# Performance work log

Measured on AMD Instinct MI355X. Metric: run time of the kernel, lower is better.

The kernel has to match this reference:

```python
import jax, jax.numpy as jnp
import numpy as np

EPS = 1e-5


def setup_inputs() -> dict:
    key = jax.random.key(0)
    ks = jax.random.split(key, 8)
    B, C, D, H, O, E = 256, 64, 256, 4096, 256, 4
    x = jax.random.normal(ks[0], (B, C, D), dtype=jnp.float32)
    mask_ids = jax.random.randint(ks[1], (B, C), 0, 16)
    projection_idx = jax.random.randint(ks[2], (C,), 0, E)
    W1 = jax.random.normal(ks[3], (E, D, H), dtype=jnp.float32) * 0.02
    b1 = jnp.zeros((E, H), dtype=jnp.float32)
    gamma = jnp.ones((E, H), dtype=jnp.float32)
    beta = jnp.zeros((E, H), dtype=jnp.float32)
    W2 = jax.random.normal(ks[4], (E, H, O), dtype=jnp.float32) * 0.02
    b2 = jnp.zeros((E, O), dtype=jnp.float32)
    return {"x": x, "mask_ids": mask_ids, "projection_idx": projection_idx,
            "W1": W1, "b1": b1, "gamma": gamma, "beta": beta, "W2": W2, "b2": b2}


def reference(x, mask_ids, projection_idx, W1, b1, gamma, beta, W2, b2):
    # x: [B, C, D]; projection_idx: [C] routes each channel to one of E experts.
    # Disjoint masks => the original zeros + masked '+=' is a partition-assign.
    B, C, D = x.shape
    E, _, H = W1.shape
    # Per-channel expert params (gather once, shared over batch).
    h = jnp.einsum('bcd,cdh->bch', x, W1[projection_idx]) + b1[projection_idx]
    # BatchNorm1d in training mode: batch stats over the tokens of each expert
    # (the original flattens the selected [B, |mask|] tokens for BN).
    seg = jnp.broadcast_to(projection_idx[None, :], (B, C)).reshape(-1)  # [B*C]
    hf = h.reshape(B * C, H)
    cnt = jax.ops.segment_sum(jnp.ones((B * C,), h.dtype), seg, num_segments=E)
    cnt = jnp.maximum(cnt, 1.0)
    s1 = jax.ops.segment_sum(hf, seg, num_segments=E)            # [E, H]
    s2 = jax.ops.segment_sum(hf * hf, seg, num_segments=E)       # [E, H]
    mean = s1 / cnt[:, None]
    var = s2 / cnt[:, None] - mean * mean                        # biased var (train-mode BN)
    inv = jax.lax.rsqrt(var + EPS)
    hn = (h - mean[projection_idx]) * (inv[projection_idx] * gamma[projection_idx]) + beta[projection_idx]
    a = jax.nn.relu(hn)
    out = jnp.einsum('bch,cho->bco', a, W2[projection_idx]) + b2[projection_idx]
    return out, mask_ids
```

## Files before the change

### kernel.cpp

```cpp
#include <hip/hip_runtime.h>

typedef unsigned short u16;
typedef unsigned int   u32;
typedef __attribute__((ext_vector_type(8))) short s16x8;
typedef __attribute__((ext_vector_type(4))) float f32x4;
typedef __attribute__((ext_vector_type(4))) u32   u32x4;

#define DEV static __device__ __forceinline__

static constexpr int B_ = 256, C_ = 64, D_ = 256, H_ = 4096, O_ = 256, E_ = 4;

DEV u16 f2bf(float f) {
  u32 u = __builtin_bit_cast(u32, f);
  u += 0x7fffu + ((u >> 16) & 1u);
  return (u16)(u >> 16);
}
DEV float bf2f(u16 u) { return __builtin_bit_cast(float, (u32)u << 16); }

DEV void async16(const u16* g, u16* l) {
  __builtin_amdgcn_global_load_lds(
      (const __attribute__((address_space(1))) void*)g,
      (__attribute__((address_space(3))) void*)l, 16, 0, 0);
}

DEV int xcd_swz(int bid, int nwg) { return (bid & 7) * (nwg >> 3) + (bid >> 3); }

__global__ void k_cvt(const float* __restrict__ src, u16* __restrict__ dst) {
  const int i = blockIdx.x * blockDim.x + threadIdx.x;
  const f32x4 a = ((const f32x4*)src)[2 * i];
  const f32x4 b = ((const f32x4*)src)[2 * i + 1];
  u32x4 o;
  o[0] = (u32)f2bf(a[0]) | ((u32)f2bf(a[1]) << 16);
  o[1] = (u32)f2bf(a[2]) | ((u32)f2bf(a[3]) << 16);
  o[2] = (u32)f2bf(b[0]) | ((u32)f2bf(b[1]) << 16);
  o[3] = (u32)f2bf(b[2]) | ((u32)f2bf(b[3]) << 16);
  ((u32x4*)dst)[i] = o;
}

__global__ void k_transpose(const float* __restrict__ src, u16* __restrict__ dst,
                            const int R, const int Cc) {
  __shared__ float tile[64][65];
  const int nct = Cc >> 6, nrt = R >> 6;
  int bx = blockIdx.x;
  const int ct = bx % nct; bx /= nct;
  const int rt = bx % nrt; const int e = bx / nrt;
  const float* s = src + (size_t)e * R * Cc;
  u16* d = dst + (size_t)e * R * Cc;
  const int tx = threadIdx.x & 63, ty = threadIdx.x >> 6;
  #pragma unroll
  for (int i = 0; i < 64; i += 4)
    tile[i + ty][tx] = s[(size_t)(rt * 64 + i + ty) * Cc + ct * 64 + tx];
  __syncthreads();
  #pragma unroll
  for (int i = 0; i < 64; i += 4) {
    const int cc = i + ty;
    d[(size_t)(ct * 64 + cc) * R + rt * 64 + tx] = f2bf(tile[tx][cc]);
  }
}

__global__ void k_sortc(const int* __restrict__ proj, int* __restrict__ perm) {
  const int c = threadIdx.x;
  const int e = proj[c];
  int rank = 0;
  for (int c2 = 0; c2 < C_; ++c2) {
    const int e2 = proj[c2];
    rank += (e2 < e) || (e2 == e && c2 < c);
  }
  perm[rank] = c;
}

__global__ __launch_bounds__(256, 4)
void k_gemm1(const u16* __restrict__ A, const u16* __restrict__ Bw,
             const int* __restrict__ proj, const int* __restrict__ perm,
             const float* __restrict__ bias,
             u16* __restrict__ outH, float* __restrict__ s1g, float* __restrict__ s2g) {
  constexpr int BM = 128, BN = 128, BK = 32, KT = D_ / BK;
  constexpr int SA = BM * BK / 8, SB = BN * BK / 8;
  constexpr int BUF = (SA + SB) * 8;
  __shared__ __align__(16) u16 lds[2 * BUF];
  const int tid = threadIdx.x, l = tid & 63, w = tid >> 6, wm = w >> 1, wn = w & 1;

  int bid = xcd_swz(blockIdx.x, gridDim.x);
  constexpr int NT = H_ / BN, BT = B_ / BM;
  const int nt = bid % NT; bid /= NT;
  const int bt = bid % BT; const int ci = bid / BT;
  const int c = perm[ci];
  const int e = proj[c];

  const size_t rsA = (size_t)C_ * D_;
  const u16* Ab = A + (size_t)c * D_ + (size_t)bt * BM * rsA;
  const u16* Bb = Bw + ((size_t)e * H_ + (size_t)nt * BN) * D_;

  f32x4 acc[4][4] = {};

  auto stage = [&](int kt) {
    const int k0 = kt * BK;
    u16* dst = lds + (kt & 1) * BUF;
    #pragma unroll
    for (int i = 0; i < SA / 256; ++i) {
      const int s = i * 256 + tid, row = s >> 2, j = (s & 3) ^ (row & 3);
      async16(Ab + (size_t)row * rsA + k0 + j * 8, dst + s * 8);
    }
    #pragma unroll
    for (int i = 0; i < SB / 256; ++i) {
      const int s = i * 256 + tid, col = s >> 2, j = (s & 3) ^ (col & 3);
      async16(Bb + (size_t)col * D_ + k0 + j * 8, dst + SA * 8 + s * 8);
    }
  };

  stage(0);
  asm volatile("s_waitcnt vmcnt(0)" ::: "memory");
  __builtin_amdgcn_s_barrier();

  #pragma unroll
  for (int kt = 0; kt < KT; ++kt) {
    if (kt + 1 < KT) stage(kt + 1);
    const u16* bufA = lds + (kt & 1) * BUF;
    const u16* bufB = bufA + SA * 8;
    s16x8 av[4], bv[4];
    #pragma unroll
    for (int m = 0; m < 4; ++m) {
      const int r = wm * 64 + m * 16 + (l & 15), p = (l >> 4) ^ (r & 3);
      av[m] = *(const s16x8*)(bufA + (r * 4 + p) * 8);
    }
    #pragma unroll
    for (int n = 0; n < 4; ++n) {
      const int cc = wn * 64 + n * 16 + (l & 15), p = (l >> 4) ^ (cc & 3);
      bv[n] = *(const s16x8*)(bufB + (cc * 4 + p) * 8);
    }
    #pragma unroll
    for (int m = 0; m < 4; ++m)
      #pragma unroll
      for (int n = 0; n < 4; ++n)
        acc[m][n] = __builtin_amdgcn_mfma_f32_16x16x32_bf16(av[m], bv[n], acc[m][n], 0, 0, 0);
    asm volatile("s_waitcnt vmcnt(0) lgkmcnt(0)" ::: "memory");
    __builtin_amdgcn_s_barrier();
  }

  u16* ldsOut = lds;
  #pragma unroll
  for (int n = 0; n < 4; ++n) {
    const int colL = wn * 64 + n * 16 + (l & 15);
    const int colg = nt * BN + colL;
    const float bval = bias[e * H_ + colg];
    float p1 = 0.f, p2 = 0.f;
    #pragma unroll
    for (int m = 0; m < 4; ++m) {
      const int rbase = wm * 64 + m * 16 + (l >> 4) * 4;
      #pragma unroll
      for (int i = 0; i < 4; ++i) {
        const float v = acc[m][n][i] + bval;
        p1 += v; p2 += v * v;
        const int row = rbase + i;
        const int phys = (colL >> 3) ^ (row & 15);
        ldsOut[row * 128 + phys * 8 + (colL & 7)] = f2bf(v);
      }
    }
    p1 += __shfl_xor(p1, 16); p1 += __shfl_xor(p1, 32);
    p2 += __shfl_xor(p2, 16); p2 += __shfl_xor(p2, 32);
    if (l < 16) {
      atomicAdd(&s1g[e * H_ + colg], p1);
      atomicAdd(&s2g[e * H_ + colg], p2);
    }
  }
  __syncthreads();
  u16* outB = outH + ((size_t)(bt * BM) * C_ + c) * H_ + nt * BN;
  #pragma unroll
  for (int pass = 0; pass < 8; ++pass) {
    const int row = pass * 16 + (tid >> 4), sl = tid & 15;
    const u32x4 v = *(const u32x4*)(ldsOut + row * 128 + ((sl ^ (row & 15)) * 8));
    *(u32x4*)(outB + (size_t)row * C_ * H_ + sl * 8) = v;
  }
}

__global__ void k_finalize(const float* __restrict__ s1, const float* __restrict__ s2,
                           const int* __restrict__ proj, const float* __restrict__ gamma,
                           const float* __restrict__ beta,
                           u16* __restrict__ sclB, u16* __restrict__ shfB) {
  const int i = blockIdx.x * 256 + threadIdx.x;
  const int e = i >> 12;
  int cn = 0;
  #pragma unroll
  for (int c = 0; c < C_; ++c) cn += (proj[c] == e) ? 1 : 0;
  const float cnt = fmaxf((float)cn * (float)B_, 1.f);
  const float mean = s1[i] / cnt;
  const float var = s2[i] / cnt - mean * mean;
  const float sc = rsqrtf(var + 1e-5f) * gamma[i];
  sclB[i] = f2bf(sc);
  shfB[i] = f2bf(beta[i] - mean * sc);
}

__global__ __launch_bounds__(256, 2)
void k_gemm2(const u16* __restrict__ A, const u16* __restrict__ Bw,
             const int* __restrict__ proj, const int* __restrict__ perm,
             const float* __restrict__ b2,
             const u16* __restrict__ scB, const u16* __restrict__ shB,
             float* __restrict__ outF, float* __restrict__ partial) {
  constexpr int BM = 128, BN = 128, BK = 64, KH = H_ / 2, KT = KH / BK;
  constexpr int SA = BM * BK / 8, SB = BN * BK / 8;
  constexpr int BUF = (SA + SB) * 8;
  __shared__ __align__(16) u16 lds[2 * BUF];
  const int tid = threadIdx.x, l = tid & 63, w = tid >> 6, wm = w >> 1, wn = w & 1;

  int bid = xcd_swz(blockIdx.x, gridDim.x);
  const int ks = bid & 1; bid >>= 1;
  const int nt = bid & 1; bid >>= 1;
  const int bt = bid & 1; const int ci = bid >> 1;
  const int c = perm[ci];
  const int e = proj[c];

  const size_t rsA = (size_t)C_ * H_;
  const u16* Ab = A + (size_t)c * H_ + (size_t)bt * BM * rsA + (size_t)ks * KH;
  const u16* Bb = Bw + ((size_t)e * O_ + (size_t)nt * BN) * H_ + (size_t)ks * KH;
  const u16* scE = scB + e * H_ + ks * KH;
  const u16* shE = shB + e * H_ + ks * KH;

  f32x4 acc[4][4] = {};
  s16x8 hA[4], sA[4], tA[4];

  auto Aissue = [&](int kt) {
    const int k0 = kt * BK;
    #pragma unroll
    for (int i = 0; i < 4; ++i) {
      const int s = i * 256 + tid, row = s >> 3, j = (s & 7) ^ (row & 7), k = k0 + j * 8;
      hA[i] = *(const s16x8*)(Ab + (size_t)row * rsA + k);
      sA[i] = *(const s16x8*)(scE + k);
      tA[i] = *(const s16x8*)(shE + k);
    }
  };
  auto Bissue = [&](int kt) {
    const int k0 = kt * BK;
    u16* dst = lds + (kt & 1) * BUF + SA * 8;
    #pragma unroll
    for (int i = 0; i < 4; ++i) {
      const int s = i * 256 + tid, col = s >> 3, j = (s & 7) ^ (col & 7);
      async16(Bb + (size_t)col * H_ + k0 + j * 8, dst + s * 8);
    }
  };
  auto Awrite = [&](int kt) {
    u16* dst = lds + (kt & 1) * BUF;
    #pragma unroll
    for (int i = 0; i < 4; ++i) {
      const int s = i * 256 + tid;
      u32x4 o;
      #pragma unroll
      for (int jj = 0; jj < 4; ++jj) {
        const float v0 = fmaxf(bf2f((u16)hA[i][2 * jj]) * bf2f((u16)sA[i][2 * jj]) + bf2f((u16)tA[i][2 * jj]), 0.f);
        const float v1 = fmaxf(bf2f((u16)hA[i][2 * jj + 1]) * bf2f((u16)sA[i][2 * jj + 1]) + bf2f((u16)tA[i][2 * jj + 1]), 0.f);
        o[jj] = (u32)f2bf(v0) | ((u32)f2bf(v1) << 16);
      }
      *(u32x4*)(dst + s * 8) = o;
    }
  };

  Aissue(0); Bissue(0); Awrite(0);
  asm volatile("s_waitcnt vmcnt(0) lgkmcnt(0)" ::: "memory");
  __builtin_amdgcn_s_barrier();

  #pragma unroll 2
  for (int kt = 0; kt < KT; ++kt) {
    if (kt + 1 < KT) { Aissue(kt + 1); Bissue(kt + 1); }
    const u16* bufA = lds + (kt & 1) * BUF;
    const u16* bufB = bufA + SA * 8;
    s16x8 av[2][4], bv[2][4];
    #pragma unroll
    for (int kk = 0; kk < 2; ++kk) {
      #pragma unroll
      for (int m = 0; m < 4; ++m) {
        const int r = wm * 64 + m * 16 + (l & 15), p = (kk * 4 + (l >> 4)) ^ (r & 7);
        av[kk][m] = *(const s16x8*)(bufA + (r * 8 + p) * 8);
      }
      #pragma unroll
      for (int n = 0; n < 4; ++n) {
        const int cc = wn * 64 + n * 16 + (l & 15), p = (kk * 4 + (l >> 4)) ^ (cc & 7);
        bv[kk][n] = *(const s16x8*)(bufB + (cc * 8 + p) * 8);
      }
    }
    #pragma unroll
    for (int kk = 0; kk < 2; ++kk)
      #pragma unroll
      for (int m = 0; m < 4; ++m)
        #pragma unroll
        for (int n = 0; n < 4; ++n)
          acc[m][n] = __builtin_amdgcn_mfma_f32_16x16x32_bf16(av[kk][m], bv[kk][n], acc[m][n], 0, 0, 0);
    if (kt + 1 < KT) Awrite(kt + 1);
    asm volatile("s_waitcnt vmcnt(0) lgkmcnt(0)" ::: "memory");
    __builtin_amdgcn_s_barrier();
  }

  float* dstF = ks ? partial : outF;
  #pragma unroll
  for (int n = 0; n < 4; ++n) {
    const int colg = nt * BN + wn * 64 + n * 16 + (l & 15);
    const float bval = ks ? 0.f : b2[e * O_ + colg];
    #pragma unroll
    for (int m = 0; m < 4; ++m) {
      #pragma unroll
      for (int i = 0; i < 4; ++i) {
        const int rg = bt * BM + wm * 64 + m * 16 + (l >> 4) * 4 + i;
        dstF[((size_t)rg * C_ + c) * O_ + colg] = acc[m][n][i] + bval;
      }
    }
  }
}

__global__ void k_combine(float* __restrict__ out, const float* __restrict__ partial,
                          const int* __restrict__ mask, float* __restrict__ maskOut) {
  const int gi = blockIdx.x * 256 + threadIdx.x;
  const size_t b = (size_t)gi * 2;
  f32x4 a0 = ((const f32x4*)out)[b],     a1 = ((const f32x4*)out)[b + 1];
  const f32x4 p0 = ((const f32x4*)partial)[b], p1 = ((const f32x4*)partial)[b + 1];
  #pragma unroll
  for (int j = 0; j < 4; ++j) { a0[j] += p0[j]; a1[j] += p1[j]; }
  ((f32x4*)out)[b] = a0; ((f32x4*)out)[b + 1] = a1;
  if (gi < B_ * C_ / 8) {
    #pragma unroll
    for (int j = 0; j < 8; ++j) maskOut[gi * 8 + j] = (float)mask[gi * 8 + j];
  }
}

extern "C" void kernel_launch(void* const* d_in, const int* in_sizes, int n_in,
                              void* d_out, int out_size, void* d_ws, size_t ws_size,
                              hipStream_t stream) {
  const float* x     = (const float*)d_in[0];
  const int*   mask  = (const int*)d_in[1];
  const int*   proj  = (const int*)d_in[2];
  const float* W1    = (const float*)d_in[3];
  const float* b1    = (const float*)d_in[4];
  const float* gamma = (const float*)d_in[5];
  const float* beta  = (const float*)d_in[6];
  const float* W2    = (const float*)d_in[7];
  const float* b2    = (const float*)d_in[8];
  float* out = (float*)d_out;

  char* ws = (char*)d_ws;
  size_t off = 0;
  u16* hbuf = (u16*)(ws + off); off += (size_t)B_ * C_ * H_ * 2;
  u16* xb   = (u16*)(ws + off); off += (size_t)B_ * C_ * D_ * 2;
  u16* w1t  = (u16*)(ws + off); off += (size_t)E_ * D_ * H_ * 2;
  float* partial = (float*)xb;
  u16* w2t  = (u16*)(ws + off); off += (size_t)E_ * H_ * O_ * 2;
  float* s1 = (float*)(ws + off); off += (size_t)E_ * H_ * 4;
  float* s2 = (float*)(ws + off); off += (size_t)E_ * H_ * 4;
  u16* sclB = (u16*)(ws + off); off += (size_t)E_ * H_ * 2;
  u16* shfB = (u16*)(ws + off); off += (size_t)E_ * H_ * 2;
  int* perm = (int*)(ws + off); off += 256;

  (void)hipMemsetAsync(s1, 0, (size_t)2 * E_ * H_ * 4, stream);

  k_sortc<<<1, 64, 0, stream>>>(proj, perm);
  k_cvt<<<2048, 256, 0, stream>>>(x, xb);
  k_transpose<<<E_ * 4 * 64, 256, 0, stream>>>(W1, w1t, D_, H_);
  k_transpose<<<E_ * 64 * 4, 256, 0, stream>>>(W2, w2t, H_, O_);

  k_gemm1<<<C_ * 2 * 32, 256, 0, stream>>>(xb, w1t, proj, perm, b1, hbuf, s1, s2);

  k_finalize<<<E_ * H_ / 256, 256, 0, stream>>>(s1, s2, proj, gamma, beta, sclB, shfB);

  k_gemm2<<<512, 256, 0, stream>>>(hbuf, w2t, proj, perm, b2, sclB, shfB, out, partial);

  k_combine<<<B_ * C_ * O_ / 8 / 256, 256, 0, stream>>>(out, partial, mask,
                                                        out + (size_t)B_ * C_ * O_);
}
```

Measured before the change: 160.3 us.

## Restructure gemm2 into triple-buffered register-staged pipeline with LDS-cached BN scale/shift

The second GEMM now uses a K tile of 32 instead of 64. LDS becomes a three-deep ring buffer. Both A and B tiles are loaded into registers two steps ahead and written to LDS one step ahead, replacing the async global-to-LDS copies for B. The BatchNorm scale and shift vectors for the block's K range are loaded into LDS once, instead of being re-read from global memory on every A load. This is meant to hide global latency behind MFMA work and cut redundant scale/shift traffic, at the cost of more barriers per K and more register pressure. The gemm1 loop bounds are hardcoded to 2, which is presumably equal to the previous constant.

```diff
diff --git a/kernel.cpp b/kernel.cpp
--- a/kernel.cpp
+++ b/kernel.cpp
@@ -97,12 +97,12 @@
     const int k0 = kt * BK;
     u16* dst = lds + (kt & 1) * BUF;
     #pragma unroll
-    for (int i = 0; i < SA / 256; ++i) {
+    for (int i = 0; i < 2; ++i) {
       const int s = i * 256 + tid, row = s >> 2, j = (s & 3) ^ (row & 3);
       async16(Ab + (size_t)row * rsA + k0 + j * 8, dst + s * 8);
     }
     #pragma unroll
-    for (int i = 0; i < SB / 256; ++i) {
+    for (int i = 0; i < 2; ++i) {
       const int s = i * 256 + tid, col = s >> 2, j = (s & 3) ^ (col & 3);
       async16(Bb + (size_t)col * D_ + k0 + j * 8, dst + SA * 8 + s * 8);
     }
@@ -196,10 +196,12 @@
              const float* __restrict__ b2,
              const u16* __restrict__ scB, const u16* __restrict__ shB,
              float* __restrict__ outF, float* __restrict__ partial) {
-  constexpr int BM = 128, BN = 128, BK = 64, KH = H_ / 2, KT = KH / BK;
+  constexpr int BM = 128, BN = 128, BK = 32, KH = H_ / 2, KT = KH / BK;
   constexpr int SA = BM * BK / 8, SB = BN * BK / 8;
   constexpr int BUF = (SA + SB) * 8;
-  __shared__ __align__(16) u16 lds[2 * BUF];
+  __shared__ __align__(16) u16 lds[3 * BUF + 2 * KH];
+  u16* stS = lds + 3 * BUF;
+  u16* stT = stS + KH;
   const int tid = threadIdx.x, l = tid & 63, w = tid >> 6, wm = w >> 1, wn = w & 1;
 
   int bid = xcd_swz(blockIdx.x, gridDim.x);
@@ -216,77 +218,99 @@
   const u16* shE = shB + e * H_ + ks * KH;
 
   f32x4 acc[4][4] = {};
-  s16x8 hA[4], sA[4], tA[4];
-
-  auto Aissue = [&](int kt) {
+  s16x8 h0[2], h1[2], b0r[2], b1r[2];
+
+  auto Aissue = [&](int kt, s16x8 (&hs)[2]) {
     const int k0 = kt * BK;
     #pragma unroll
-    for (int i = 0; i < 4; ++i) {
-      const int s = i * 256 + tid, row = s >> 3, j = (s & 7) ^ (row & 7), k = k0 + j * 8;
-      hA[i] = *(const s16x8*)(Ab + (size_t)row * rsA + k);
-      sA[i] = *(const s16x8*)(scE + k);
-      tA[i] = *(const s16x8*)(shE + k);
-    }
-  };
-  auto Bissue = [&](int kt) {
+    for (int i = 0; i < 2; ++i) {
+      const int s = i * 256 + tid, row = s >> 2, j = (s & 3) ^ (row & 3);
+      hs[i] = *(const s16x8*)(Ab + (size_t)row * rsA + k0 + j * 8);
+    }
+  };
+  auto Bissue = [&](int kt, s16x8 (&bs)[2]) {
     const int k0 = kt * BK;
-    u16* dst = lds + (kt & 1) * BUF + SA * 8;
-    #pragma unroll
-    for (int i = 0; i < 4; ++i) {
-      const int s = i * 256 + tid, col = s >> 3, j = (s & 7) ^ (col & 7);
-      async16(Bb + (size_t)col * H_ + k0 + j * 8, dst + s * 8);
-    }
-  };
-  auto Awrite = [&](int kt) {
-    u16* dst = lds + (kt & 1) * BUF;
-    #pragma unroll
-    for (int i = 0; i < 4; ++i) {
-      const int s = i * 256 + tid;
+    #pragma unroll
+    for (int i = 0; i < 2; ++i) {
+      const int s = i * 256 + tid, col = s >> 2, j = (s & 3) ^ (col & 3);
+      bs[i] = *(const s16x8*)(Bb + (size_t)col * H_ + k0 + j * 8);
+    }
+  };
+  auto Awrite = [&](int kt, s16x8 (&hs)[2]) {
+    u16* dst = lds + (kt % 3) * BUF;
+    const int k0 = kt * BK;
+    #pragma unroll
+    for (int i = 0; i < 2; ++i) {
+      const int s = i * 256 + tid, row = s >> 2, j = (s & 3) ^ (row & 3);
+      const s16x8 sv = *(const s16x8*)(stS + k0 + j * 8);
+      const s16x8 tv = *(const s16x8*)(stT + k0 + j * 8);
       u32x4 o;
       #pragma unroll
       for (int jj = 0; jj < 4; ++jj) {
-        const float v0 = fmaxf(bf2f((u16)hA[i][2 * jj]) * bf2f((u16)sA[i][2 * jj]) + bf2f((u16)tA[i][2 * jj]), 0.f);
-        const float v1 = fmaxf(bf2f((u16)hA[i][2 * jj + 1]) * bf2f((u16)sA[i][2 * jj + 1]) + bf2f((u16)tA[i][2 * jj + 1]), 0.f);
+        const float v0 = fmaxf(bf2f((u16)hs[i][2 * jj]) * bf2f((u16)sv[2 * jj]) + bf2f((u16)tv[2 * jj]), 0.f);
+        const float v1 = fmaxf(bf2f((u16)hs[i][2 * jj + 1]) * bf2f((u16)sv[2 * jj + 1]) + bf2f((u16)tv[2 * jj + 1]), 0.f);
         o[jj] = (u32)f2bf(v0) | ((u32)f2bf(v1) << 16);
       }
       *(u32x4*)(dst + s * 8) = o;
     }
   };
-
-  Aissue(0); Bissue(0); Awrite(0);
-  asm volatile("s_waitcnt vmcnt(0) lgkmcnt(0)" ::: "memory");
+  auto Bwrite = [&](int kt, s16x8 (&bs)[2]) {
+    u16* dst = lds + (kt % 3) * BUF + SA * 8;
+    #pragma unroll
+    for (int i = 0; i < 2; ++i) {
+      const int s = i * 256 + tid;
+      *(u32x4*)(dst + s * 8) = __builtin_bit_cast(u32x4, bs[i]);
+    }
+  };
+  auto Compute = [&](int kt) {
+    const u16* bufA = lds + (kt % 3) * BUF;
+    const u16* bufB = bufA + SA * 8;
+    s16x8 av[4], bv[4];
+    #pragma unroll
+    for (int m = 0; m < 4; ++m) {
+      const int r = wm * 64 + m * 16 + (l & 15), p = (l >> 4) ^ (r & 3);
+      av[m] = *(const s16x8*)(bufA + (r * 4 + p) * 8);
+    }
+    #pragma unroll
+    for (int n = 0; n < 4; ++n) {
+      const int cc = wn * 64 + n * 16 + (l & 15), p = (l >> 4) ^ (cc & 3);
+      bv[n] = *(const s16x8*)(bufB + (cc * 4 + p) * 8);
+    }
+    #pragma unroll
+    for (int m = 0; m < 4; ++m)
+      #pragma unroll
+      for (int n = 0; n < 4; ++n)
+        acc[m][n] = __builtin_amdgcn_mfma_f32_16x16x32_bf16(av[m], bv[n], acc[m][n], 0, 0, 0);
+  };
+
+  async16(scE + tid * 8, stS + tid * 8);
+  async16(shE + tid * 8, stT + tid * 8);
+  Aissue(0, h0); Bissue(0, b0r);
+  Aissue(1, h1); Bissue(1, b1r);
+  asm volatile("s_waitcnt vmcnt(0)" ::: "memory");
+  Awrite(0, h0); Bwrite(0, b0r);
+  asm volatile("s_waitcnt lgkmcnt(0)" ::: "memory");
   __builtin_amdgcn_s_barrier();
 
-  #pragma unroll 2
-  for (int kt = 0; kt < KT; ++kt) {
-    if (kt + 1 < KT) { Aissue(kt + 1); Bissue(kt + 1); }
-    const u16* bufA = lds + (kt & 1) * BUF;
-    const u16* bufB = bufA + SA * 8;
-    s16x8 av[2][4], bv[2][4];
-    #pragma unroll
-    for (int kk = 0; kk < 2; ++kk) {
-      #pragma unroll
-      for (int m = 0; m < 4; ++m) {
-        const int r = wm * 64 + m * 16 + (l & 15), p = (kk * 4 + (l >> 4)) ^ (r & 7);
-        av[kk][m] = *(const s16x8*)(bufA + (r * 8 + p) * 8);
-      }
-      #pragma unroll
-      for (int n = 0; n < 4; ++n) {
-        const int cc = wn * 64 + n * 16 + (l & 15), p = (kk * 4 + (l >> 4)) ^ (cc & 7);
-        bv[kk][n] = *(const s16x8*)(bufB + (cc * 8 + p) * 8);
-      }
-    }
-    #pragma unroll
-    for (int kk = 0; kk < 2; ++kk)
-      #pragma unroll
-      for (int m = 0; m < 4; ++m)
-        #pragma unroll
-        for (int n = 0; n < 4; ++n)
-          acc[m][n] = __builtin_amdgcn_mfma_f32_16x16x32_bf16(av[kk][m], bv[kk][n], acc[m][n], 0, 0, 0);
-    if (kt + 1 < KT) Awrite(kt + 1);
-    asm volatile("s_waitcnt vmcnt(0) lgkmcnt(0)" ::: "memory");
+  #pragma unroll 1
+  for (int kt = 0; kt + 3 < KT; kt += 2) {
+    Aissue(kt + 2, h0); Bissue(kt + 2, b0r);
+    Awrite(kt + 1, h1); Bwrite(kt + 1, b1r);
+    Compute(kt);
+    asm volatile("s_waitcnt lgkmcnt(0)" ::: "memory");
     __builtin_amdgcn_s_barrier();
-  }
+    Aissue(kt + 3, h1); Bissue(kt + 3, b1r);
+    Awrite(kt + 2, h0); Bwrite(kt + 2, b0r);
+    Compute(kt + 1);
+    asm volatile("s_waitcnt lgkmcnt(0)" ::: "memory");
+    __builtin_amdgcn_s_barrier();
+  }
+
+  Awrite(KT - 1, h1); Bwrite(KT - 1, b1r);
+  Compute(KT - 2);
+  asm volatile("s_waitcnt lgkmcnt(0)" ::: "memory");
+  __builtin_amdgcn_s_barrier();
+  Compute(KT - 1);
 
   float* dstF = ks ? partial : outF;
   #pragma unroll
```

After: 160.1 us. No clear change (-0.2%).
